# Performance work log

Measured on AMD Instinct MI355X. Metric: run time of the kernel, lower is better.

## Reference

```python
import jax, jax.numpy as jnp
import numpy as np

K = 64          # number of tags, incl. BOS/EOS
V = 50000       # vocab size (excl. BOS/EOS words)
D = 128         # lexicon embedding dim
BOS_T = K - 2   # BOS tag index
EOS_T = K - 1   # EOS tag index
BATCH = 8192
L = 126         # interior words per sentence (n = L + 2 incl. BOS/EOS)
EPS = 1e-45     # smoothing added to A and B in updateAB


def setup_inputs() -> dict:
    key = jax.random.key(0)
    k1, k2, k3, k4 = jax.random.split(key, 4)
    words = jax.random.randint(k1, (BATCH, L), 0, V, dtype=jnp.int32)
    ThetaB = 0.01 * jax.random.uniform(k2, (K, D), dtype=jnp.float32)
    WA = 0.01 * jax.random.uniform(k3, (K, K), dtype=jnp.float32)
    E = jax.random.normal(k4, (V, D), dtype=jnp.float32)
    return {"words": words, "ThetaB": ThetaB, "WA": WA, "E": E}


def reference(words, ThetaB, WA, E):
    # updateAB(): A = softmax(WA) with BOS column forced to prob 0 (-inf logit)
    WAm = WA.at[:, BOS_T].set(-jnp.inf)
    A = jax.nn.softmax(WAm, axis=1) + EPS                       # [K, K]
    B = jax.nn.softmax(ThetaB @ E.T, axis=1)                    # [K, V]
    B = B.at[EOS_T, :].set(0.0).at[BOS_T, :].set(0.0) + EPS
    logA = jnp.log(A)                                           # [K, K]
    logB = jnp.log(B)                                           # [K, V]

    # Emission log-probs gathered per token: [L, B, K]
    em = jnp.swapaxes(logB.T[words], 0, 1)

    # alpha_0: one-hot (in log space) at BOS tag
    alpha0 = jnp.full((words.shape[0], K), -jnp.inf, dtype=logA.dtype)
    alpha0 = alpha0.at[:, BOS_T].set(0.0)

    def step(alpha, e):
        # alpha: [B, K] over prev tags; logsumexp over prev tag axis
        new = jax.nn.logsumexp(alpha[:, :, None] + logA[None, :, :], axis=1) + e
        return new, None

    alpha, _ = jax.lax.scan(step, alpha0, em)
    # Final transition into EOS tag (no emission): log Z per sentence, [B]
    logZ = jax.nn.logsumexp(alpha + logA[None, :, EOS_T], axis=1)
    return logZ
```

## Files before the change

### kernel.cpp

```cpp
#include <hip/hip_runtime.h>
#include <hip/hip_bf16.h>
#include <math.h>


#define KT 64
#define VV 50000
#define DD 128
#define BOS_T 62
#define EOS_T 63
#define LLEN 126
#define EPSF 1e-45f
#define SCALE_F 65536.0f
#define LOG_TOTAL_SCALE (2016.0f * 0.6931471805599453f)
#define NBLK 782
#define PBLK 784
#define TPH 21
#define NPH 6

#define BTN_OFF   0
#define A_OFF     3200000
#define SUM_OFF   3216384
#define PART_OFF  3216640

typedef short short8 __attribute__((ext_vector_type(8)));
typedef float f32x4  __attribute__((ext_vector_type(4)));
typedef float f32x2  __attribute__((ext_vector_type(2)));

union U8 { short8 v; unsigned u[4]; short s[8]; };

static __device__ inline unsigned short f2bf_u(float x) {
    __hip_bfloat16 h = __float2bfloat16(x);
    return *reinterpret_cast<unsigned short*>(&h);
}
static __device__ inline short f2bf(float x) { return (short)f2bf_u(x); }

#if __has_builtin(__builtin_amdgcn_cvt_pk_bf16_f32)
typedef __bf16 bf16x2 __attribute__((ext_vector_type(2)));
static __device__ inline unsigned pk2(float a, float b) {
    bf16x2 r = __builtin_amdgcn_cvt_pk_bf16_f32(a, b);
    return *reinterpret_cast<unsigned*>(&r);
}
#else
static __device__ inline unsigned pk2(float a, float b) {
    union { float f; unsigned u; } ua, ub;
    ua.f = a; ub.f = b;
    return ((ua.u + 0x8000u) >> 16) | ((ub.u + 0x8000u) & 0xFFFF0000u);
}
#endif
static __device__ inline float lo16(unsigned u) { union { unsigned i; float f; } c; c.i = u << 16;        return c.f; }
static __device__ inline float hi16(unsigned u) { union { unsigned i; float f; } c; c.i = u & 0xffff0000u; return c.f; }

#if __has_builtin(__builtin_amdgcn_cvt_pk_fp8_f32)
static __device__ inline unsigned pk4f8(float a, float b, float c, float d) {
    int v = __builtin_amdgcn_cvt_pk_fp8_f32(a, b, 0, false);
    v = __builtin_amdgcn_cvt_pk_fp8_f32(c, d, v, true);
    return (unsigned)v;
}
#else
static __device__ inline unsigned enc1f8(float x) {
    union { float f; unsigned u; } c; c.f = x;
    unsigned u = c.u & 0x7FFFFFFFu;
    unsigned r = u + 0x7FFFFu + ((u >> 20) & 1u);
    return ((r >> 20) - (120u << 3)) & 0x7Fu;
}
static __device__ inline unsigned pk4f8(float a, float b, float c, float d) {
    return enc1f8(a) | (enc1f8(b) << 8) | (enc1f8(c) << 16) | (enc1f8(d) << 24);
}
#endif

#if __has_builtin(__builtin_amdgcn_cvt_pk_f32_fp8)
static __device__ inline f32x2 dec2lo(unsigned w) { return __builtin_amdgcn_cvt_pk_f32_fp8((int)w, false); }
static __device__ inline f32x2 dec2hi(unsigned w) { return __builtin_amdgcn_cvt_pk_f32_fp8((int)w, true); }
#else
static __device__ inline float dec1f8(unsigned b) {
    union { unsigned u; float f; } c;
    c.u = ((b & 0x80u) << 24) | (((b & 0x7Fu) << 20) + (120u << 23));
    return c.f;
}
static __device__ inline f32x2 dec2lo(unsigned w) { f32x2 r; r.x = dec1f8(w & 0xFF); r.y = dec1f8((w >> 8) & 0xFF); return r; }
static __device__ inline f32x2 dec2hi(unsigned w) { f32x2 r; r.x = dec1f8((w >> 16) & 0xFF); r.y = dec1f8(w >> 24); return r; }
#endif

#if __has_builtin(__builtin_amdgcn_global_load_lds)
#define GLLDS(gp, lbase)                                                        \
    __builtin_amdgcn_global_load_lds(                                           \
        (__attribute__((address_space(1))) void*)const_cast<unsigned char*>(gp),\
        (__attribute__((address_space(3))) void*)(lbase), 16, 0, 0)
#else
#define GLLDS(gp, lbase)                                                        \
    do { *(uint4*)((unsigned char*)(lbase) + (threadIdx.x & 63) * 16) =         \
             *(const uint4*)(gp); } while (0)
#endif

__global__ __launch_bounds__(256) void k_emit(const float* __restrict__ ThetaB,
                                              const float* __restrict__ E,
                                              unsigned char* __restrict__ btn8,
                                              float* __restrict__ partial) {
    __shared__ float red[4][KT];
    int t    = threadIdx.x;
    int lane = t & 63;
    int w    = t >> 6;
    int n    = lane & 15;
    int q    = lane >> 4;
    int v0   = (blockIdx.x * 4 + w) * 16;

    int rowE = v0 + n;
    bool valid = rowE < VV;
    rowE = valid ? rowE : VV - 1;
    float4 ex[4][2];
#pragma unroll
    for (int kt = 0; kt < 4; ++kt) {
        const float* p = E + (size_t)rowE * DD + kt * 32 + q * 8;
        ex[kt][0] = *(const float4*)p;
        ex[kt][1] = *(const float4*)(p + 4);
    }

    short8 Th[4][4];
#pragma unroll
    for (int kt = 0; kt < 4; ++kt)
#pragma unroll
        for (int mt = 0; mt < 4; ++mt) {
            const float* p = ThetaB + (mt * 16 + n) * DD + kt * 32 + q * 8;
            float4 x = *(const float4*)p;
            float4 y = *(const float4*)(p + 4);
            U8 f;
            f.u[0] = pk2(x.x, x.y); f.u[1] = pk2(x.z, x.w);
            f.u[2] = pk2(y.x, y.y); f.u[3] = pk2(y.z, y.w);
            Th[kt][mt] = f.v;
        }

    short8 Ef[4];
#pragma unroll
    for (int kt = 0; kt < 4; ++kt) {
        U8 f;
        f.u[0] = pk2(ex[kt][0].x, ex[kt][0].y); f.u[1] = pk2(ex[kt][0].z, ex[kt][0].w);
        f.u[2] = pk2(ex[kt][1].x, ex[kt][1].y); f.u[3] = pk2(ex[kt][1].z, ex[kt][1].w);
        Ef[kt] = f.v;
    }

#pragma unroll
    for (int mt = 0; mt < 4; ++mt) {
        f32x4 C = {0.f, 0.f, 0.f, 0.f};
#pragma unroll
        for (int kt = 0; kt < 4; ++kt)
            C = __builtin_amdgcn_mfma_f32_16x16x32_bf16(Th[kt][mt], Ef[kt], C, 0, 0, 0);
        float e[4];
#pragma unroll
        for (int r = 0; r < 4; ++r) e[r] = __expf(C[r]);
        if (valid) {
            int pos = 16 * ((2 * mt + (q >> 1)) & 3) + 8 * (mt >> 1) + (q & 1) * 4;
            *(unsigned*)(btn8 + (size_t)rowE * KT + pos) = pk4f8(e[0], e[1], e[2], e[3]);
        }
#pragma unroll
        for (int r = 0; r < 4; ++r) {
            float s = valid ? e[r] : 0.0f;
            s += __shfl_xor(s, 1, 64);
            s += __shfl_xor(s, 2, 64);
            s += __shfl_xor(s, 4, 64);
            s += __shfl_xor(s, 8, 64);
            if (n == 0) red[w][mt * 16 + q * 4 + r] = s;
        }
    }
    __syncthreads();
    if (w == 0) {
        float s = red[0][lane] + red[1][lane] + red[2][lane] + red[3][lane];
        partial[lane * PBLK + blockIdx.x] = s;
    }
}

__global__ __launch_bounds__(256) void k_sumA(const float* __restrict__ partial,
                                              const float* __restrict__ WA,
                                              float* __restrict__ sumexp,
                                              float* __restrict__ A) {
    __shared__ float r[4];
    int k = blockIdx.x;
    int t = threadIdx.x;
    float s = 0.0f;
    for (int i = t; i < NBLK; i += 256) s += partial[k * PBLK + i];
#pragma unroll
    for (int off = 32; off > 0; off >>= 1) s += __shfl_xor(s, off, 64);
    if ((t & 63) == 0) r[t >> 6] = s;
    __syncthreads();
    if (t == 0) sumexp[k] = r[0] + r[1] + r[2] + r[3];
    if (t < 64) {
        float wv = WA[k * KT + t];
        float e = (t == BOS_T) ? 0.0f : __expf(wv);
        float se = e;
#pragma unroll
        for (int off = 32; off > 0; off >>= 1) se += __shfl_xor(se, off, 64);
        A[k * KT + t] = e / se + EPSF;
    }
}

__global__ __launch_bounds__(256) void k_fwd(const int* __restrict__ words,
                                             const unsigned char* __restrict__ btn8,
                                             const float* __restrict__ A,
                                             const float* __restrict__ sumexp,
                                             float* __restrict__ out) {
    __shared__ int shw[16 * LLEN];
    __shared__ __attribute__((aligned(16))) unsigned char shE[2][TPH * 1024];
    int lane = threadIdx.x & 63;
    int w    = threadIdx.x >> 6;
    int n    = lane & 15;
    int qA   = lane >> 4;
    int b0   = blockIdx.x * 16;

    {
        const uint4* src = (const uint4*)(words + (size_t)b0 * LLEN);
        uint4* dst = (uint4*)shw;
        for (int idx = threadIdx.x; idx < (16 * LLEN) / 4; idx += 256)
            dst[idx] = src[idx];
    }

    short8 Af[2][4];
    short8 B0, B1;
    if (w == 3) {
#pragma unroll
        for (int mt = 0; mt < 4; ++mt) {
            int tagn = 32 * (mt >> 1) + 8 * (n >> 2) + 4 * (mt & 1) + (n & 3);
            float s = sumexp[tagn];
            float rsn = (tagn == BOS_T || tagn == EOS_T) ? 0.0f : (SCALE_F / s);
#pragma unroll
            for (int kt = 0; kt < 2; ++kt) {
                U8 f;
#pragma unroll
                for (int j = 0; j < 8; ++j)
                    f.s[j] = f2bf(A[(kt * 32 + qA * 8 + j) * KT + tagn] * rsn);
                Af[kt][mt] = f.v;
            }
        }
        U8 z; z.u[0] = z.u[1] = z.u[2] = z.u[3] = 0;
        B0 = z.v;
        U8 o; o.u[0] = o.u[1] = o.u[2] = o.u[3] = 0;
        if (qA == 3) o.s[6] = (short)0x3F80;
        B1 = o.v;
    }
    __syncthreads();

#define PSTAGE(bb, p_)                                                        \
    do {                                                                      \
        for (int s_ = w; s_ < TPH; s_ += 3) {                                 \
            int wd_ = shw[n * LLEN + (p_) * TPH + s_];                        \
            const unsigned char* g_ = btn8 + (size_t)wd_ * KT + qA * 16;      \
            GLLDS(g_, &shE[bb][s_ * 1024]);                                   \
        }                                                                     \
        asm volatile("s_waitcnt vmcnt(0)" ::: "memory");                      \
    } while (0)

#define LDE(bb, ss) (*(const uint4*)(&shE[bb][(ss) * 1024] + lane * 16))

    if (w < 3) PSTAGE(0, 0);
    __syncthreads();

    for (int p = 0; p < NPH; ++p) {
        int b = p & 1;
        if (w < 3) {
            if (p + 1 < NPH) PSTAGE((p + 1) & 1, p + 1);
        } else {
            uint4 r0 = LDE(b, 0);
            uint4 r1 = LDE(b, 1);
#pragma unroll
            for (int s = 0; s < TPH; ++s) {
                uint4 rc = r0;
                r0 = r1;
                int s2 = (s + 2 < TPH) ? s + 2 : TPH - 1;
                r1 = LDE(b, s2);

                f32x2 d0 = dec2lo(rc.x), d1 = dec2hi(rc.x);
                f32x2 d2 = dec2lo(rc.y), d3 = dec2hi(rc.y);
                f32x2 d4 = dec2lo(rc.z), d5 = dec2hi(rc.z);
                f32x2 d6 = dec2lo(rc.w), d7 = dec2hi(rc.w);

                f32x4 C[4];
#pragma unroll
                for (int mt = 0; mt < 4; ++mt) {
                    f32x4 acc = {0.f, 0.f, 0.f, 0.f};
                    acc = __builtin_amdgcn_mfma_f32_16x16x32_bf16(Af[0][mt], B0, acc, 0, 0, 0);
                    acc = __builtin_amdgcn_mfma_f32_16x16x32_bf16(Af[1][mt], B1, acc, 0, 0, 0);
                    C[mt] = acc;
                }
                U8 f0, f1;
                f0.u[0] = pk2(C[0][0] * d0.x, C[0][1] * d0.y);
                f0.u[1] = pk2(C[0][2] * d1.x, C[0][3] * d1.y);
                f0.u[2] = pk2(C[1][0] * d2.x, C[1][1] * d2.y);
                f0.u[3] = pk2(C[1][2] * d3.x, C[1][3] * d3.y);
                f1.u[0] = pk2(C[2][0] * d4.x, C[2][1] * d4.y);
                f1.u[1] = pk2(C[2][2] * d5.x, C[2][3] * d5.y);
                f1.u[2] = pk2(C[3][0] * d6.x, C[3][1] * d6.y);
                f1.u[3] = pk2(C[3][2] * d7.x, C[3][3] * d7.y);
                B0 = f0.v; B1 = f1.v;
            }
        }
        __syncthreads();
    }

    if (w == 3) {
        short8 Afin[2];
#pragma unroll
        for (int kt = 0; kt < 2; ++kt) {
            U8 f;
#pragma unroll
            for (int j = 0; j < 8; ++j)
                f.s[j] = (n == 0) ? f2bf(A[(kt * 32 + qA * 8 + j) * KT + EOS_T]) : (short)0;
            Afin[kt] = f.v;
        }
        f32x4 Cf = {0.f, 0.f, 0.f, 0.f};
        Cf = __builtin_amdgcn_mfma_f32_16x16x32_bf16(Afin[0], B0, Cf, 0, 0, 0);
        Cf = __builtin_amdgcn_mfma_f32_16x16x32_bf16(Afin[1], B1, Cf, 0, 0, 0);
        if (qA == 0)
            out[b0 + n] = logf(Cf[0]) - LOG_TOTAL_SCALE;
    }
}

extern "C" void kernel_launch(void* const* d_in, const int* in_sizes, int n_in,
                              void* d_out, int out_size, void* d_ws, size_t ws_size,
                              hipStream_t stream) {
    const int*   words  = (const int*)d_in[0];
    const float* ThetaB = (const float*)d_in[1];
    const float* WA     = (const float*)d_in[2];
    const float* E      = (const float*)d_in[3];
    float* out = (float*)d_out;

    char* ws = (char*)d_ws;
    unsigned char* btn8 = (unsigned char*)(ws + BTN_OFF);
    float* A       = (float*)(ws + A_OFF);
    float* sumexp  = (float*)(ws + SUM_OFF);
    float* partial = (float*)(ws + PART_OFF);

    k_emit<<<NBLK, 256, 0, stream>>>(ThetaB, E, btn8, partial);
    k_sumA<<<KT, 256, 0, stream>>>(partial, WA, sumexp, A);
    k_fwd<<<8192 / 16, 256, 0, stream>>>(words, btn8, A, sumexp, out);
}
```

Before: 128.0 us.

## Fuse three kernels into one persistent kernel with software grid barriers

Merges the emission, normalisation and forward kernels into one persistent launch of 512 blocks, separated by two atomic grid-wide barriers, and loads the word indices into LDS before the emission phase. The aim is to remove two kernel launch gaps and their tail effects. In exchange it adds a memset launch and spin-barrier cost. It relies on all 512 blocks being resident at once; otherwise the barrier would deadlock.

```diff
diff --git a/kernel.cpp b/kernel.cpp
--- a/kernel.cpp
+++ b/kernel.cpp
@@ -16,11 +16,13 @@
 #define PBLK 784
 #define TPH 21
 #define NPH 6
+#define GRIDN 512
 
 #define BTN_OFF   0
 #define A_OFF     3200000
 #define SUM_OFF   3216384
 #define PART_OFF  3216640
+#define BAR_OFF   3417344
 
 typedef short short8 __attribute__((ext_vector_type(8)));
 typedef float f32x4  __attribute__((ext_vector_type(4)));
@@ -47,8 +49,6 @@
     return ((ua.u + 0x8000u) >> 16) | ((ub.u + 0x8000u) & 0xFFFF0000u);
 }
 #endif
-static __device__ inline float lo16(unsigned u) { union { unsigned i; float f; } c; c.i = u << 16;        return c.f; }
-static __device__ inline float hi16(unsigned u) { union { unsigned i; float f; } c; c.i = u & 0xffff0000u; return c.f; }
 
 #if __has_builtin(__builtin_amdgcn_cvt_pk_fp8_f32)
 static __device__ inline unsigned pk4f8(float a, float b, float c, float d) {
@@ -92,27 +92,50 @@
              *(const uint4*)(gp); } while (0)
 #endif
 
-__global__ __launch_bounds__(256) void k_emit(const float* __restrict__ ThetaB,
-                                              const float* __restrict__ E,
-                                              unsigned char* __restrict__ btn8,
-                                              float* __restrict__ partial) {
+static __device__ inline void grid_barrier(unsigned* bar, unsigned nblk) {
+    __syncthreads();
+    if (threadIdx.x == 0) {
+        unsigned* cnt = bar;
+        unsigned* gen = bar + 16;
+        unsigned g = __hip_atomic_load(gen, __ATOMIC_RELAXED, __HIP_MEMORY_SCOPE_AGENT);
+        unsigned a = __hip_atomic_fetch_add(cnt, 1u, __ATOMIC_ACQ_REL, __HIP_MEMORY_SCOPE_AGENT);
+        if (a == nblk - 1u) {
+            __hip_atomic_store(cnt, 0u, __ATOMIC_RELAXED, __HIP_MEMORY_SCOPE_AGENT);
+            __hip_atomic_fetch_add(gen, 1u, __ATOMIC_RELEASE, __HIP_MEMORY_SCOPE_AGENT);
+        } else {
+            while (__hip_atomic_load(gen, __ATOMIC_RELAXED, __HIP_MEMORY_SCOPE_AGENT) == g)
+                __builtin_amdgcn_s_sleep(2);
+            __builtin_amdgcn_fence(__ATOMIC_ACQUIRE, "agent");
+        }
+    }
+    __syncthreads();
+}
+
+__global__ __launch_bounds__(256, 2) void k_fused(const int* __restrict__ words,
+                                                  const float* __restrict__ ThetaB,
+                                                  const float* __restrict__ WA,
+                                                  const float* __restrict__ E,
+                                                  unsigned char* __restrict__ btn8,
+                                                  float* __restrict__ partial,
+                                                  float* __restrict__ sumexp,
+                                                  float* __restrict__ A,
+                                                  float* __restrict__ out,
+                                                  unsigned* __restrict__ bar) {
     __shared__ float red[4][KT];
+    __shared__ int shw[16 * LLEN];
+    __shared__ __attribute__((aligned(16))) unsigned char shE[2][TPH * 1024];
+
     int t    = threadIdx.x;
     int lane = t & 63;
     int w    = t >> 6;
     int n    = lane & 15;
     int q    = lane >> 4;
-    int v0   = (blockIdx.x * 4 + w) * 16;
-
-    int rowE = v0 + n;
-    bool valid = rowE < VV;
-    rowE = valid ? rowE : VV - 1;
-    float4 ex[4][2];
-#pragma unroll
-    for (int kt = 0; kt < 4; ++kt) {
-        const float* p = E + (size_t)rowE * DD + kt * 32 + q * 8;
-        ex[kt][0] = *(const float4*)p;
-        ex[kt][1] = *(const float4*)(p + 4);
+
+    {
+        const uint4* src = (const uint4*)(words + (size_t)(blockIdx.x * 16) * LLEN);
+        uint4* dst = (uint4*)shw;
+        for (int idx = t; idx < (16 * LLEN) / 4; idx += 256)
+            dst[idx] = src[idx];
     }
 
     short8 Th[4][4];
@@ -129,113 +152,87 @@
             Th[kt][mt] = f.v;
         }
 
-    short8 Ef[4];
-#pragma unroll
-    for (int kt = 0; kt < 4; ++kt) {
-        U8 f;
-        f.u[0] = pk2(ex[kt][0].x, ex[kt][0].y); f.u[1] = pk2(ex[kt][0].z, ex[kt][0].w);
-        f.u[2] = pk2(ex[kt][1].x, ex[kt][1].y); f.u[3] = pk2(ex[kt][1].z, ex[kt][1].w);
-        Ef[kt] = f.v;
-    }
-
-#pragma unroll
-    for (int mt = 0; mt < 4; ++mt) {
-        f32x4 C = {0.f, 0.f, 0.f, 0.f};
-#pragma unroll
-        for (int kt = 0; kt < 4; ++kt)
-            C = __builtin_amdgcn_mfma_f32_16x16x32_bf16(Th[kt][mt], Ef[kt], C, 0, 0, 0);
-        float e[4];
-#pragma unroll
-        for (int r = 0; r < 4; ++r) e[r] = __expf(C[r]);
-        if (valid) {
-            int pos = 16 * ((2 * mt + (q >> 1)) & 3) + 8 * (mt >> 1) + (q & 1) * 4;
-            *(unsigned*)(btn8 + (size_t)rowE * KT + pos) = pk4f8(e[0], e[1], e[2], e[3]);
-        }
-#pragma unroll
-        for (int r = 0; r < 4; ++r) {
-            float s = valid ? e[r] : 0.0f;
-            s += __shfl_xor(s, 1, 64);
-            s += __shfl_xor(s, 2, 64);
-            s += __shfl_xor(s, 4, 64);
-            s += __shfl_xor(s, 8, 64);
-            if (n == 0) red[w][mt * 16 + q * 4 + r] = s;
-        }
-    }
-    __syncthreads();
-    if (w == 0) {
-        float s = red[0][lane] + red[1][lane] + red[2][lane] + red[3][lane];
-        partial[lane * PBLK + blockIdx.x] = s;
-    }
-}
-
-__global__ __launch_bounds__(256) void k_sumA(const float* __restrict__ partial,
-                                              const float* __restrict__ WA,
-                                              float* __restrict__ sumexp,
-                                              float* __restrict__ A) {
-    __shared__ float r[4];
-    int k = blockIdx.x;
-    int t = threadIdx.x;
-    float s = 0.0f;
-    for (int i = t; i < NBLK; i += 256) s += partial[k * PBLK + i];
-#pragma unroll
-    for (int off = 32; off > 0; off >>= 1) s += __shfl_xor(s, off, 64);
-    if ((t & 63) == 0) r[t >> 6] = s;
-    __syncthreads();
-    if (t == 0) sumexp[k] = r[0] + r[1] + r[2] + r[3];
-    if (t < 64) {
-        float wv = WA[k * KT + t];
-        float e = (t == BOS_T) ? 0.0f : __expf(wv);
-        float se = e;
-#pragma unroll
-        for (int off = 32; off > 0; off >>= 1) se += __shfl_xor(se, off, 64);
-        A[k * KT + t] = e / se + EPSF;
-    }
-}
-
-__global__ __launch_bounds__(256) void k_fwd(const int* __restrict__ words,
-                                             const unsigned char* __restrict__ btn8,
-                                             const float* __restrict__ A,
-                                             const float* __restrict__ sumexp,
-                                             float* __restrict__ out) {
-    __shared__ int shw[16 * LLEN];
-    __shared__ __attribute__((aligned(16))) unsigned char shE[2][TPH * 1024];
-    int lane = threadIdx.x & 63;
-    int w    = threadIdx.x >> 6;
-    int n    = lane & 15;
-    int qA   = lane >> 4;
-    int b0   = blockIdx.x * 16;
-
-    {
-        const uint4* src = (const uint4*)(words + (size_t)b0 * LLEN);
-        uint4* dst = (uint4*)shw;
-        for (int idx = threadIdx.x; idx < (16 * LLEN) / 4; idx += 256)
-            dst[idx] = src[idx];
-    }
+    for (int tile = blockIdx.x; tile < NBLK; tile += GRIDN) {
+        int v0   = (tile * 4 + w) * 16;
+        int rowE = v0 + n;
+        bool valid = rowE < VV;
+        rowE = valid ? rowE : VV - 1;
+
+        float4 ex[4][2];
+#pragma unroll
+        for (int kt = 0; kt < 4; ++kt) {
+            const float* p = E + (size_t)rowE * DD + kt * 32 + q * 8;
+            ex[kt][0] = *(const float4*)p;
+            ex[kt][1] = *(const float4*)(p + 4);
+        }
+        short8 Ef[4];
+#pragma unroll
+        for (int kt = 0; kt < 4; ++kt) {
+            U8 f;
+            f.u[0] = pk2(ex[kt][0].x, ex[kt][0].y); f.u[1] = pk2(ex[kt][0].z, ex[kt][0].w);
+            f.u[2] = pk2(ex[kt][1].x, ex[kt][1].y); f.u[3] = pk2(ex[kt][1].z, ex[kt][1].w);
+            Ef[kt] = f.v;
+        }
+
+#pragma unroll
+        for (int mt = 0; mt < 4; ++mt) {
+            f32x4 C = {0.f, 0.f, 0.f, 0.f};
+#pragma unroll
+            for (int kt = 0; kt < 4; ++kt)
+                C = __builtin_amdgcn_mfma_f32_16x16x32_bf16(Th[kt][mt], Ef[kt], C, 0, 0, 0);
+            float e[4];
+#pragma unroll
+            for (int r = 0; r < 4; ++r) e[r] = __expf(C[r]);
+            if (valid) {
+                int pos = 16 * ((2 * mt + (q >> 1)) & 3) + 8 * (mt >> 1) + (q & 1) * 4;
+                *(unsigned*)(btn8 + (size_t)rowE * KT + pos) = pk4f8(e[0], e[1], e[2], e[3]);
+            }
+#pragma unroll
+            for (int r = 0; r < 4; ++r) {
+                float s = valid ? e[r] : 0.0f;
+                s += __shfl_xor(s, 1, 64);
+                s += __shfl_xor(s, 2, 64);
+                s += __shfl_xor(s, 4, 64);
+                s += __shfl_xor(s, 8, 64);
+                if (n == 0) red[w][mt * 16 + q * 4 + r] = s;
+            }
+        }
+        __syncthreads();
+        if (w == 0) {
+            float s = red[0][lane] + red[1][lane] + red[2][lane] + red[3][lane];
+            partial[lane * PBLK + tile] = s;
+        }
+        __syncthreads();
+    }
+
+    grid_barrier(bar, GRIDN);
+
+    if (blockIdx.x < KT) {
+        int k = blockIdx.x;
+        float s = 0.0f;
+        for (int i = t; i < NBLK; i += 256) s += partial[k * PBLK + i];
+#pragma unroll
+        for (int off = 32; off > 0; off >>= 1) s += __shfl_xor(s, off, 64);
+        if ((t & 63) == 0) red[0][t >> 6] = s;
+        __syncthreads();
+        if (t == 0) sumexp[k] = red[0][0] + red[0][1] + red[0][2] + red[0][3];
+        if (t < 64) {
+            float wv = WA[k * KT + t];
+            float e = (t == BOS_T) ? 0.0f : __expf(wv);
+            float se = e;
+#pragma unroll
+            for (int off = 32; off > 0; off >>= 1) se += __shfl_xor(se, off, 64);
+            A[k * KT + t] = e / se + EPSF;
+        }
+    }
+
+    grid_barrier(bar, GRIDN);
+
+    int b0 = blockIdx.x * 16;
+    int qA = q;
 
     short8 Af[2][4];
     short8 B0, B1;
-    if (w == 3) {
-#pragma unroll
-        for (int mt = 0; mt < 4; ++mt) {
-            int tagn = 32 * (mt >> 1) + 8 * (n >> 2) + 4 * (mt & 1) + (n & 3);
-            float s = sumexp[tagn];
-            float rsn = (tagn == BOS_T || tagn == EOS_T) ? 0.0f : (SCALE_F / s);
-#pragma unroll
-            for (int kt = 0; kt < 2; ++kt) {
-                U8 f;
-#pragma unroll
-                for (int j = 0; j < 8; ++j)
-                    f.s[j] = f2bf(A[(kt * 32 + qA * 8 + j) * KT + tagn] * rsn);
-                Af[kt][mt] = f.v;
-            }
-        }
-        U8 z; z.u[0] = z.u[1] = z.u[2] = z.u[3] = 0;
-        B0 = z.v;
-        U8 o; o.u[0] = o.u[1] = o.u[2] = o.u[3] = 0;
-        if (qA == 3) o.s[6] = (short)0x3F80;
-        B1 = o.v;
-    }
-    __syncthreads();
 
 #define PSTAGE(bb, p_)                                                        \
     do {                                                                      \
@@ -249,7 +246,29 @@
 
 #define LDE(bb, ss) (*(const uint4*)(&shE[bb][(ss) * 1024] + lane * 16))
 
-    if (w < 3) PSTAGE(0, 0);
+    if (w < 3) {
+        PSTAGE(0, 0);
+    } else {
+#pragma unroll
+        for (int mt = 0; mt < 4; ++mt) {
+            int tagn = 32 * (mt >> 1) + 8 * (n >> 2) + 4 * (mt & 1) + (n & 3);
+            float s = sumexp[tagn];
+            float rsn = (tagn == BOS_T || tagn == EOS_T) ? 0.0f : (SCALE_F / s);
+#pragma unroll
+            for (int kt = 0; kt < 2; ++kt) {
+                U8 f;
+#pragma unroll
+                for (int j = 0; j < 8; ++j)
+                    f.s[j] = f2bf(A[(kt * 32 + qA * 8 + j) * KT + tagn] * rsn);
+                Af[kt][mt] = f.v;
+            }
+        }
+        U8 z; z.u[0] = z.u[1] = z.u[2] = z.u[3] = 0;
+        B0 = z.v;
+        U8 o; o.u[0] = o.u[1] = o.u[2] = o.u[3] = 0;
+        if (qA == 3) o.s[6] = (short)0x3F80;
+        B1 = o.v;
+    }
     __syncthreads();
 
     for (int p = 0; p < NPH; ++p) {
@@ -310,6 +329,8 @@
         if (qA == 0)
             out[b0 + n] = logf(Cf[0]) - LOG_TOTAL_SCALE;
     }
+#undef PSTAGE
+#undef LDE
 }
 
 extern "C" void kernel_launch(void* const* d_in, const int* in_sizes, int n_in,
@@ -323,11 +344,12 @@
 
     char* ws = (char*)d_ws;
     unsigned char* btn8 = (unsigned char*)(ws + BTN_OFF);
-    float* A       = (float*)(ws + A_OFF);
-    float* sumexp  = (float*)(ws + SUM_OFF);
-    float* partial = (float*)(ws + PART_OFF);
-
-    k_emit<<<NBLK, 256, 0, stream>>>(ThetaB, E, btn8, partial);
-    k_sumA<<<KT, 256, 0, stream>>>(partial, WA, sumexp, A);
-    k_fwd<<<8192 / 16, 256, 0, stream>>>(words, btn8, A, sumexp, out);
-}
+    float* A        = (float*)(ws + A_OFF);
+    float* sumexp   = (float*)(ws + SUM_OFF);
+    float* partial  = (float*)(ws + PART_OFF);
+    unsigned* bar   = (unsigned*)(ws + BAR_OFF);
+
+    hipMemsetAsync(ws + BAR_OFF, 0, 128, stream);
+    k_fused<<<GRIDN, 256, 0, stream>>>(words, ThetaB, WA, E, btn8, partial,
+                                       sumexp, A, out, bar);
+}
```

Result: slower. 189.6 us (+48.1%).

## Fold sumA into emit atomics and scan kernel, compute A in LDS

Applied to the files above, without the earlier changes.

Drops the k_sumA launch. Per-block emission sums are now combined with atomicAdd into a zeroed sumexp buffer. Each forward block recomputes the transition softmax A from WA into shared memory. This removes one kernel launch, the partial buffer round-trip and global reads of A. In exchange it adds a memset, 64-way atomic contention across 782 blocks, 16KB more LDS per block (possible occupancy change) and redundant A computation in every block.

```diff
diff --git a/kernel.cpp b/kernel.cpp
--- a/kernel.cpp
+++ b/kernel.cpp
@@ -13,14 +13,12 @@
 #define SCALE_F 65536.0f
 #define LOG_TOTAL_SCALE (2016.0f * 0.6931471805599453f)
 #define NBLK 782
-#define PBLK 784
 #define TPH 21
 #define NPH 6
+#define GRIDN 512
 
 #define BTN_OFF   0
-#define A_OFF     3200000
 #define SUM_OFF   3216384
-#define PART_OFF  3216640
 
 typedef short short8 __attribute__((ext_vector_type(8)));
 typedef float f32x4  __attribute__((ext_vector_type(4)));
@@ -47,8 +45,6 @@
     return ((ua.u + 0x8000u) >> 16) | ((ub.u + 0x8000u) & 0xFFFF0000u);
 }
 #endif
-static __device__ inline float lo16(unsigned u) { union { unsigned i; float f; } c; c.i = u << 16;        return c.f; }
-static __device__ inline float hi16(unsigned u) { union { unsigned i; float f; } c; c.i = u & 0xffff0000u; return c.f; }
 
 #if __has_builtin(__builtin_amdgcn_cvt_pk_fp8_f32)
 static __device__ inline unsigned pk4f8(float a, float b, float c, float d) {
@@ -95,7 +91,7 @@
 __global__ __launch_bounds__(256) void k_emit(const float* __restrict__ ThetaB,
                                               const float* __restrict__ E,
                                               unsigned char* __restrict__ btn8,
-                                              float* __restrict__ partial) {
+                                              float* __restrict__ sumexp) {
     __shared__ float red[4][KT];
     int t    = threadIdx.x;
     int lane = t & 63;
@@ -164,39 +160,16 @@
     __syncthreads();
     if (w == 0) {
         float s = red[0][lane] + red[1][lane] + red[2][lane] + red[3][lane];
-        partial[lane * PBLK + blockIdx.x] = s;
-    }
-}
-
-__global__ __launch_bounds__(256) void k_sumA(const float* __restrict__ partial,
+        atomicAdd(sumexp + lane, s);
+    }
+}
+
+__global__ __launch_bounds__(256) void k_scan(const int* __restrict__ words,
                                               const float* __restrict__ WA,
-                                              float* __restrict__ sumexp,
-                                              float* __restrict__ A) {
-    __shared__ float r[4];
-    int k = blockIdx.x;
-    int t = threadIdx.x;
-    float s = 0.0f;
-    for (int i = t; i < NBLK; i += 256) s += partial[k * PBLK + i];
-#pragma unroll
-    for (int off = 32; off > 0; off >>= 1) s += __shfl_xor(s, off, 64);
-    if ((t & 63) == 0) r[t >> 6] = s;
-    __syncthreads();
-    if (t == 0) sumexp[k] = r[0] + r[1] + r[2] + r[3];
-    if (t < 64) {
-        float wv = WA[k * KT + t];
-        float e = (t == BOS_T) ? 0.0f : __expf(wv);
-        float se = e;
-#pragma unroll
-        for (int off = 32; off > 0; off >>= 1) se += __shfl_xor(se, off, 64);
-        A[k * KT + t] = e / se + EPSF;
-    }
-}
-
-__global__ __launch_bounds__(256) void k_fwd(const int* __restrict__ words,
-                                             const unsigned char* __restrict__ btn8,
-                                             const float* __restrict__ A,
-                                             const float* __restrict__ sumexp,
-                                             float* __restrict__ out) {
+                                              const unsigned char* __restrict__ btn8,
+                                              const float* __restrict__ sumexp,
+                                              float* __restrict__ out) {
+    __shared__ float A_lds[KT][KT];
     __shared__ int shw[16 * LLEN];
     __shared__ __attribute__((aligned(16))) unsigned char shE[2][TPH * 1024];
     int lane = threadIdx.x & 63;
@@ -212,6 +185,17 @@
             dst[idx] = src[idx];
     }
 
+    for (int rr = 0; rr < 16; ++rr) {
+        int row = w * 16 + rr;
+        float wv = WA[row * KT + lane];
+        float e = (lane == BOS_T) ? 0.0f : __expf(wv);
+        float se = e;
+#pragma unroll
+        for (int off = 32; off > 0; off >>= 1) se += __shfl_xor(se, off, 64);
+        A_lds[row][lane] = e / se + EPSF;
+    }
+    __syncthreads();
+
     short8 Af[2][4];
     short8 B0, B1;
     if (w == 3) {
@@ -225,7 +209,7 @@
                 U8 f;
 #pragma unroll
                 for (int j = 0; j < 8; ++j)
-                    f.s[j] = f2bf(A[(kt * 32 + qA * 8 + j) * KT + tagn] * rsn);
+                    f.s[j] = f2bf(A_lds[kt * 32 + qA * 8 + j][tagn] * rsn);
                 Af[kt][mt] = f.v;
             }
         }
@@ -235,7 +219,6 @@
         if (qA == 3) o.s[6] = (short)0x3F80;
         B1 = o.v;
     }
-    __syncthreads();
 
 #define PSTAGE(bb, p_)                                                        \
     do {                                                                      \
@@ -301,7 +284,7 @@
             U8 f;
 #pragma unroll
             for (int j = 0; j < 8; ++j)
-                f.s[j] = (n == 0) ? f2bf(A[(kt * 32 + qA * 8 + j) * KT + EOS_T]) : (short)0;
+                f.s[j] = (n == 0) ? f2bf(A_lds[kt * 32 + qA * 8 + j][EOS_T]) : (short)0;
             Afin[kt] = f.v;
         }
         f32x4 Cf = {0.f, 0.f, 0.f, 0.f};
@@ -310,6 +293,8 @@
         if (qA == 0)
             out[b0 + n] = logf(Cf[0]) - LOG_TOTAL_SCALE;
     }
+#undef PSTAGE
+#undef LDE
 }
 
 extern "C" void kernel_launch(void* const* d_in, const int* in_sizes, int n_in,
@@ -323,11 +308,9 @@
 
     char* ws = (char*)d_ws;
     unsigned char* btn8 = (unsigned char*)(ws + BTN_OFF);
-    float* A       = (float*)(ws + A_OFF);
-    float* sumexp  = (float*)(ws + SUM_OFF);
-    float* partial = (float*)(ws + PART_OFF);
-
-    k_emit<<<NBLK, 256, 0, stream>>>(ThetaB, E, btn8, partial);
-    k_sumA<<<KT, 256, 0, stream>>>(partial, WA, sumexp, A);
-    k_fwd<<<8192 / 16, 256, 0, stream>>>(words, btn8, A, sumexp, out);
-}
+    float* sumexp = (float*)(ws + SUM_OFF);
+
+    hipMemsetAsync(ws + SUM_OFF, 0, KT * sizeof(float), stream);
+    k_emit<<<NBLK, 256, 0, stream>>>(ThetaB, E, btn8, sumexp);
+    k_scan<<<GRIDN, 256, 0, stream>>>(words, WA, btn8, sumexp, out);
+}
```

After: 145.4 us. +13.6%, slower.

## Replace producer-warp LDS staging with single-wave register prefetch pipeline

Applied to the files above, without the earlier changes.

The forward scan kernel drops its three producer waves that staged emission rows into LDS through global_load_lds with block barriers. Each block is now a single 64-lane wave that prefetches emission rows straight into registers nine steps ahead, in a rotating buffer, while the MFMA recurrence runs. This removes the per-phase __syncthreads and the LDS round trip, and needs less shared memory per block. In exchange, each block has only one wave to hide latency, there are more registers per thread, and global-load latency must be covered by the prefetch depth alone.

```diff
diff --git a/kernel.cpp b/kernel.cpp
--- a/kernel.cpp
+++ b/kernel.cpp
@@ -14,8 +14,8 @@
 #define LOG_TOTAL_SCALE (2016.0f * 0.6931471805599453f)
 #define NBLK 782
 #define PBLK 784
-#define TPH 21
-#define NPH 6
+#define PFD 9
+#define ROUNDS (LLEN / PFD)
 
 #define BTN_OFF   0
 #define A_OFF     3200000
@@ -47,8 +47,6 @@
     return ((ua.u + 0x8000u) >> 16) | ((ub.u + 0x8000u) & 0xFFFF0000u);
 }
 #endif
-static __device__ inline float lo16(unsigned u) { union { unsigned i; float f; } c; c.i = u << 16;        return c.f; }
-static __device__ inline float hi16(unsigned u) { union { unsigned i; float f; } c; c.i = u & 0xffff0000u; return c.f; }
 
 #if __has_builtin(__builtin_amdgcn_cvt_pk_fp8_f32)
 static __device__ inline unsigned pk4f8(float a, float b, float c, float d) {
@@ -79,17 +77,6 @@
 }
 static __device__ inline f32x2 dec2lo(unsigned w) { f32x2 r; r.x = dec1f8(w & 0xFF); r.y = dec1f8((w >> 8) & 0xFF); return r; }
 static __device__ inline f32x2 dec2hi(unsigned w) { f32x2 r; r.x = dec1f8((w >> 16) & 0xFF); r.y = dec1f8(w >> 24); return r; }
-#endif
-
-#if __has_builtin(__builtin_amdgcn_global_load_lds)
-#define GLLDS(gp, lbase)                                                        \
-    __builtin_amdgcn_global_load_lds(                                           \
-        (__attribute__((address_space(1))) void*)const_cast<unsigned char*>(gp),\
-        (__attribute__((address_space(3))) void*)(lbase), 16, 0, 0)
-#else
-#define GLLDS(gp, lbase)                                                        \
-    do { *(uint4*)((unsigned char*)(lbase) + (threadIdx.x & 63) * 16) =         \
-             *(const uint4*)(gp); } while (0)
 #endif
 
 __global__ __launch_bounds__(256) void k_emit(const float* __restrict__ ThetaB,
@@ -192,15 +179,13 @@
     }
 }
 
-__global__ __launch_bounds__(256) void k_fwd(const int* __restrict__ words,
-                                             const unsigned char* __restrict__ btn8,
-                                             const float* __restrict__ A,
-                                             const float* __restrict__ sumexp,
-                                             float* __restrict__ out) {
+__global__ __launch_bounds__(64) void k_scan2(const int* __restrict__ words,
+                                              const unsigned char* __restrict__ btn8,
+                                              const float* __restrict__ A,
+                                              const float* __restrict__ sumexp,
+                                              float* __restrict__ out) {
     __shared__ int shw[16 * LLEN];
-    __shared__ __attribute__((aligned(16))) unsigned char shE[2][TPH * 1024];
-    int lane = threadIdx.x & 63;
-    int w    = threadIdx.x >> 6;
+    int lane = threadIdx.x;
     int n    = lane & 15;
     int qA   = lane >> 4;
     int b0   = blockIdx.x * 16;
@@ -208,27 +193,30 @@
     {
         const uint4* src = (const uint4*)(words + (size_t)b0 * LLEN);
         uint4* dst = (uint4*)shw;
-        for (int idx = threadIdx.x; idx < (16 * LLEN) / 4; idx += 256)
-            dst[idx] = src[idx];
+#pragma unroll
+        for (int it = 0; it < 8; ++it) {
+            int idx = it * 64 + lane;
+            if (idx < (16 * LLEN) / 4) dst[idx] = src[idx];
+        }
     }
 
     short8 Af[2][4];
+#pragma unroll
+    for (int mt = 0; mt < 4; ++mt) {
+        int tagn = 32 * (mt >> 1) + 8 * (n >> 2) + 4 * (mt & 1) + (n & 3);
+        float s = sumexp[tagn];
+        float rsn = (tagn == BOS_T || tagn == EOS_T) ? 0.0f : (SCALE_F / s);
+#pragma unroll
+        for (int kt = 0; kt < 2; ++kt) {
+            U8 f;
+#pragma unroll
+            for (int j = 0; j < 8; ++j)
+                f.s[j] = f2bf(A[(kt * 32 + qA * 8 + j) * KT + tagn] * rsn);
+            Af[kt][mt] = f.v;
+        }
+    }
     short8 B0, B1;
-    if (w == 3) {
-#pragma unroll
-        for (int mt = 0; mt < 4; ++mt) {
-            int tagn = 32 * (mt >> 1) + 8 * (n >> 2) + 4 * (mt & 1) + (n & 3);
-            float s = sumexp[tagn];
-            float rsn = (tagn == BOS_T || tagn == EOS_T) ? 0.0f : (SCALE_F / s);
-#pragma unroll
-            for (int kt = 0; kt < 2; ++kt) {
-                U8 f;
-#pragma unroll
-                for (int j = 0; j < 8; ++j)
-                    f.s[j] = f2bf(A[(kt * 32 + qA * 8 + j) * KT + tagn] * rsn);
-                Af[kt][mt] = f.v;
-            }
-        }
+    {
         U8 z; z.u[0] = z.u[1] = z.u[2] = z.u[3] = 0;
         B0 = z.v;
         U8 o; o.u[0] = o.u[1] = o.u[2] = o.u[3] = 0;
@@ -237,64 +225,55 @@
     }
     __syncthreads();
 
-#define PSTAGE(bb, p_)                                                        \
-    do {                                                                      \
-        for (int s_ = w; s_ < TPH; s_ += 3) {                                 \
-            int wd_ = shw[n * LLEN + (p_) * TPH + s_];                        \
-            const unsigned char* g_ = btn8 + (size_t)wd_ * KT + qA * 16;      \
-            GLLDS(g_, &shE[bb][s_ * 1024]);                                   \
-        }                                                                     \
-        asm volatile("s_waitcnt vmcnt(0)" ::: "memory");                      \
-    } while (0)
-
-#define LDE(bb, ss) (*(const uint4*)(&shE[bb][(ss) * 1024] + lane * 16))
-
-    if (w < 3) PSTAGE(0, 0);
-    __syncthreads();
-
-    for (int p = 0; p < NPH; ++p) {
-        int b = p & 1;
-        if (w < 3) {
-            if (p + 1 < NPH) PSTAGE((p + 1) & 1, p + 1);
-        } else {
-            uint4 r0 = LDE(b, 0);
-            uint4 r1 = LDE(b, 1);
-#pragma unroll
-            for (int s = 0; s < TPH; ++s) {
-                uint4 rc = r0;
-                r0 = r1;
-                int s2 = (s + 2 < TPH) ? s + 2 : TPH - 1;
-                r1 = LDE(b, s2);
-
-                f32x2 d0 = dec2lo(rc.x), d1 = dec2hi(rc.x);
-                f32x2 d2 = dec2lo(rc.y), d3 = dec2hi(rc.y);
-                f32x2 d4 = dec2lo(rc.z), d5 = dec2hi(rc.z);
-                f32x2 d6 = dec2lo(rc.w), d7 = dec2hi(rc.w);
-
-                f32x4 C[4];
-#pragma unroll
-                for (int mt = 0; mt < 4; ++mt) {
-                    f32x4 acc = {0.f, 0.f, 0.f, 0.f};
-                    acc = __builtin_amdgcn_mfma_f32_16x16x32_bf16(Af[0][mt], B0, acc, 0, 0, 0);
-                    acc = __builtin_amdgcn_mfma_f32_16x16x32_bf16(Af[1][mt], B1, acc, 0, 0, 0);
-                    C[mt] = acc;
-                }
-                U8 f0, f1;
-                f0.u[0] = pk2(C[0][0] * d0.x, C[0][1] * d0.y);
-                f0.u[1] = pk2(C[0][2] * d1.x, C[0][3] * d1.y);
-                f0.u[2] = pk2(C[1][0] * d2.x, C[1][1] * d2.y);
-                f0.u[3] = pk2(C[1][2] * d3.x, C[1][3] * d3.y);
-                f1.u[0] = pk2(C[2][0] * d4.x, C[2][1] * d4.y);
-                f1.u[1] = pk2(C[2][2] * d5.x, C[2][3] * d5.y);
-                f1.u[2] = pk2(C[3][0] * d6.x, C[3][1] * d6.y);
-                f1.u[3] = pk2(C[3][2] * d7.x, C[3][3] * d7.y);
-                B0 = f0.v; B1 = f1.v;
+    const int wrow = n * LLEN;
+
+    uint4 pf[PFD];
+    int   wdn[PFD];
+#pragma unroll
+    for (int j = 0; j < PFD; ++j) {
+        int wd = shw[wrow + j];
+        pf[j] = *(const uint4*)(btn8 + (size_t)wd * KT + qA * 16);
+    }
+#pragma unroll
+    for (int j = 0; j < PFD; ++j)
+        wdn[j] = shw[wrow + PFD + j];
+
+    for (int r = 0; r < ROUNDS; ++r) {
+#pragma unroll
+        for (int j = 0; j < PFD; ++j) {
+            uint4 rc = pf[j];
+            pf[j] = *(const uint4*)(btn8 + (size_t)wdn[j] * KT + qA * 16);
+            int s18 = r * PFD + j + 2 * PFD;
+            s18 = s18 < LLEN ? s18 : LLEN - 1;
+            wdn[j] = shw[wrow + s18];
+
+            f32x2 d0 = dec2lo(rc.x), d1 = dec2hi(rc.x);
+            f32x2 d2 = dec2lo(rc.y), d3 = dec2hi(rc.y);
+            f32x2 d4 = dec2lo(rc.z), d5 = dec2hi(rc.z);
+            f32x2 d6 = dec2lo(rc.w), d7 = dec2hi(rc.w);
+
+            f32x4 C[4];
+#pragma unroll
+            for (int mt = 0; mt < 4; ++mt) {
+                f32x4 acc = {0.f, 0.f, 0.f, 0.f};
+                acc = __builtin_amdgcn_mfma_f32_16x16x32_bf16(Af[0][mt], B0, acc, 0, 0, 0);
+                acc = __builtin_amdgcn_mfma_f32_16x16x32_bf16(Af[1][mt], B1, acc, 0, 0, 0);
+                C[mt] = acc;
             }
-        }
-        __syncthreads();
-    }
-
-    if (w == 3) {
+            U8 f0, f1;
+            f0.u[0] = pk2(C[0][0] * d0.x, C[0][1] * d0.y);
+            f0.u[1] = pk2(C[0][2] * d1.x, C[0][3] * d1.y);
+            f0.u[2] = pk2(C[1][0] * d2.x, C[1][1] * d2.y);
+            f0.u[3] = pk2(C[1][2] * d3.x, C[1][3] * d3.y);
+            f1.u[0] = pk2(C[2][0] * d4.x, C[2][1] * d4.y);
+            f1.u[1] = pk2(C[2][2] * d5.x, C[2][3] * d5.y);
+            f1.u[2] = pk2(C[3][0] * d6.x, C[3][1] * d6.y);
+            f1.u[3] = pk2(C[3][2] * d7.x, C[3][3] * d7.y);
+            B0 = f0.v; B1 = f1.v;
+        }
+    }
+
+    {
         short8 Afin[2];
 #pragma unroll
         for (int kt = 0; kt < 2; ++kt) {
@@ -329,5 +308,5 @@
 
     k_emit<<<NBLK, 256, 0, stream>>>(ThetaB, E, btn8, partial);
     k_sumA<<<KT, 256, 0, stream>>>(partial, WA, sumexp, A);
-    k_fwd<<<8192 / 16, 256, 0, stream>>>(words, btn8, A, sumexp, out);
-}
+    k_scan2<<<8192 / 16, 64, 0, stream>>>(words, btn8, A, sumexp, out);
+}
```

Result: no change. 130.0 us (+1.6%).
